# Kernel tuning notes

Hardware: AMD Instinct MI355X
Metric: run time of the kernel (lower is better)

The kernel has to match this reference:

```python
import jax, jax.numpy as jnp
import numpy as np

N, E = 50000, 800000
IN_F, OUT_F, EMB, KER = 64, 64, 3, 4


def setup_inputs() -> dict:
    key = jax.random.key(0)
    ks = jax.random.split(key, 6)
    x = jax.random.normal(ks[0], (N, IN_F), dtype=jnp.float32)
    edge_idx = jax.random.randint(ks[1], (2, E), 0, N, dtype=jnp.int64)
    spec_domain = jax.random.normal(ks[2], (N, EMB), dtype=jnp.float32)
    weight = 0.1 * jax.random.normal(ks[3], (IN_F, OUT_F, KER), dtype=jnp.float32)
    bias_p = 0.1 * jax.random.normal(ks[4], (OUT_F,), dtype=jnp.float32)
    mu = 0.005 * jax.random.normal(ks[5], (EMB, KER), dtype=jnp.float32)
    sig = jnp.ones((1, KER), dtype=jnp.float32)  # repo default 60140 underflows exp with random embeddings
    return {"x": x, "edge_idx": edge_idx, "spec_domain": spec_domain,
            "weight": weight, "bias_p": bias_p, "mu": mu, "sig": sig}


def reference(x, edge_idx, spec_domain, weight, bias_p, mu, sig):
    n = x.shape[0]
    row, col = edge_idx[0], edge_idx[1]
    # support for all kernels at once: [N, out, K]
    support = jnp.einsum('ni,iok->nok', x, weight)
    # per-edge Gaussian kernel values: [E, K]
    diff = spec_domain[row] - spec_domain[col]               # [E, emb]
    dm = diff[:, :, None] - mu[None, :, :]                   # [E, emb, K]
    qq = -0.5 * jnp.sum(dm * dm, axis=1)                     # [E, K]
    value = jnp.exp(sig[0][None, :] * qq)                    # [E, K]
    # sparse mm: out[row] += value * support[col], per kernel
    msgs = value[:, None, :] * support[col]                  # [E, out, K]
    out = jax.ops.segment_sum(msgs, row, num_segments=n)     # [N, out, K]
    return out.sum(axis=2) + bias_p
```

## Files before the change

### kernel.cpp

```cpp
#include <hip/hip_runtime.h>
#include <hip/hip_fp16.h>

#define FIN 64
#define CAP 64
#define BINSH 8
#define NBINMAX 256
#define PCAP 5120

__global__ __launch_bounds__(256) void p1_kernel(const float* __restrict__ x,
                                                 const float* __restrict__ weight,
                                                 __half* __restrict__ sup,
                                                 const int* __restrict__ eidx,
                                                 int* __restrict__ gcur,
                                                 int* __restrict__ part,
                                                 int n, int e_total) {
    const int t = threadIdx.x;
    __shared__ float xs[32][64];
    __shared__ int hist[NBINMAX], lbase[NBINMAX], gbase[NBINMAX];
    __shared__ int wsum[4];
    __shared__ int slds[512];

    const int rowbase = blockIdx.x * 32;
    if (rowbase < n) {
        {
            const float4* __restrict__ x4 = (const float4*)(x + (size_t)rowbase * 64);
            float4* __restrict__ s4 = (float4*)&xs[0][0];
            int limit = (n - rowbase) * 16;
            if (limit > 512) limit = 512;
            #pragma unroll
            for (int j = 0; j < 2; ++j) {
                int idx = t + j * 256;
                if (idx < limit) s4[idx] = x4[idx];
            }
        }
        __syncthreads();

        const int w = t >> 6;
        const int o = t & 63;

        float4 acc[8];
        #pragma unroll
        for (int r = 0; r < 8; ++r) acc[r] = make_float4(0.f, 0.f, 0.f, 0.f);

        #pragma unroll 4
        for (int ic = 0; ic < 16; ++ic) {
            float4 w0 = *(const float4*)&weight[(ic * 4 + 0) * 256 + o * 4];
            float4 w1 = *(const float4*)&weight[(ic * 4 + 1) * 256 + o * 4];
            float4 w2 = *(const float4*)&weight[(ic * 4 + 2) * 256 + o * 4];
            float4 w3 = *(const float4*)&weight[(ic * 4 + 3) * 256 + o * 4];
            #pragma unroll
            for (int r = 0; r < 8; ++r) {
                float4 xv = *(const float4*)&xs[w * 8 + r][ic * 4];
                acc[r].x += xv.x * w0.x + xv.y * w1.x + xv.z * w2.x + xv.w * w3.x;
                acc[r].y += xv.x * w0.y + xv.y * w1.y + xv.z * w2.y + xv.w * w3.y;
                acc[r].z += xv.x * w0.z + xv.y * w1.z + xv.z * w2.z + xv.w * w3.z;
                acc[r].w += xv.x * w0.w + xv.y * w1.w + xv.z * w2.w + xv.w * w3.w;
            }
        }

        #pragma unroll
        for (int r = 0; r < 8; ++r) {
            int gr = rowbase + w * 8 + r;
            if (gr < n) {
                union { __half2 h[2]; uint2 u; } p;
                p.h[0] = __floats2half2_rn(acc[r].x, acc[r].y);
                p.h[1] = __floats2half2_rn(acc[r].z, acc[r].w);
                *(uint2*)&sup[(size_t)gr * 256 + o * 4] = p.u;
            }
        }
    }

    int nz = 0;
    #pragma unroll
    for (int j = 1; j < 16; j += 2) nz |= eidx[j];
    const int is64 = (nz == 0);

    hist[t] = 0;
    __syncthreads();

    const int base = blockIdx.x * 512;
    const int nv = (e_total - base < 512) ? (e_total - base < 0 ? 0 : e_total - base)
                                          : 512;
    const int p = (base >> 1) + t;
    int r0 = 0, c0 = 0, r1 = 0, c1 = 0, v0 = 0, v1 = 0;
    if (nv > 0) {
        if (is64) {
            if (2 * t < nv) {
                int4 rr = ((const int4*)eidx)[p];
                int4 cc = ((const int4*)(eidx + 2 * (size_t)e_total))[p];
                r0 = rr.x; c0 = cc.x; v0 = 1;
                if (2 * t + 1 < nv) { r1 = rr.z; c1 = cc.z; v1 = 1; }
            }
        } else {
            if (2 * t < nv) {
                int2 rr = ((const int2*)eidx)[p];
                int2 cc = ((const int2*)(eidx + (size_t)e_total))[p];
                r0 = rr.x; c0 = cc.x; v0 = 1;
                if (2 * t + 1 < nv) { r1 = rr.y; c1 = cc.y; v1 = 1; }
            }
        }
    }
    const int b0 = r0 >> BINSH, b1 = r1 >> BINSH;
    int lp0 = 0, lp1 = 0;
    if (v0) lp0 = atomicAdd(&hist[b0], 1);
    if (v1) lp1 = atomicAdd(&hist[b1], 1);
    __syncthreads();

    {
        const int lane = t & 63;
        const int w = t >> 6;
        int h = hist[t];
        int s = h;
        #pragma unroll
        for (int off = 1; off < 64; off <<= 1) {
            int u = __shfl_up(s, off, 64);
            if (lane >= off) s += u;
        }
        if (lane == 63) wsum[w] = s;
        __syncthreads();
        if (t == 0) {
            int a = 0;
            #pragma unroll
            for (int q = 0; q < 4; ++q) { int u = wsum[q]; wsum[q] = a; a += u; }
        }
        __syncthreads();
        int ex = s - h + wsum[w];
        lbase[t] = ex;
        gbase[t] = (h > 0) ? atomicAdd(&gcur[t], h) : 0;
    }
    __syncthreads();

    if (v0) slds[lbase[b0] + lp0] = (b0 << 24) | (c0 << 8) | (r0 & 255);
    if (v1) slds[lbase[b1] + lp1] = (b1 << 24) | (c1 << 8) | (r1 & 255);
    __syncthreads();

    #pragma unroll
    for (int j = 0; j < 2; ++j) {
        int idx = t + j * 256;
        if (idx < nv) {
            int wv = slds[idx];
            int b = ((unsigned)wv) >> 24;
            int dst = gbase[b] + (idx - lbase[b]);
            if (dst < PCAP) part[b * PCAP + dst] = wv & 0x00FFFFFF;
        }
    }
}

__global__ __launch_bounds__(1024) void p2_kernel(const int* __restrict__ gcur,
                                                  const int* __restrict__ part,
                                                  int* __restrict__ cnt,
                                                  int* __restrict__ scol, int n) {
    __shared__ int cl[256];
    const int t = threadIdx.x;
    const int b = blockIdx.x;
    const int row0 = b << BINSH;
    if (t < 256) cl[t] = 0;
    __syncthreads();

    int nloc = gcur[b];
    if (nloc > PCAP) nloc = PCAP;
    const int* __restrict__ mypart = part + b * PCAP;

    for (int i = t; i < nloc; i += 1024) {
        int e = mypart[i];
        int rl = e & 255;
        int col = ((unsigned)e) >> 8;
        int pos = atomicAdd(&cl[rl], 1);
        if (pos < CAP) scol[(size_t)(row0 + rl) * CAP + pos] = col;
    }
    __syncthreads();

    int row = row0 + t;
    if (t < 256 && row < n) cnt[row] = cl[t];
}

__device__ __forceinline__ float dot_sup(uint2 p, float4 v) {
    float2 f0 = __half22float2(__builtin_bit_cast(__half2, p.x));
    float2 f1 = __half22float2(__builtin_bit_cast(__half2, p.y));
    return f0.x * v.x + f0.y * v.y + f1.x * v.z + f1.y * v.w;
}

__global__ __launch_bounds__(256, 8) void row_kernel(const int* __restrict__ cnt,
                                                     const int* __restrict__ scol,
                                                     const float* __restrict__ spec,
                                                     const float* __restrict__ mu,
                                                     const float* __restrict__ sig,
                                                     const __half* __restrict__ sup,
                                                     const float* __restrict__ bias,
                                                     float* __restrict__ out, int n) {
    __shared__ float vlds[4][64];
    const int lane = threadIdx.x & 63;
    const int wl = threadIdx.x >> 6;
    const int wv = __builtin_amdgcn_readfirstlane(blockIdx.x * 4 + wl);
    const int NW = gridDim.x * 4;

    const int k  = lane & 3;
    const int es = lane >> 2;
    const float mu0 = mu[k], mu1 = mu[4 + k], mu2 = mu[8 + k];
    const float sgk = sig[k];
    const float bias_l = bias[lane];
    const unsigned un = (unsigned)n;

    for (int r = wv; r < n; r += NW) {
        int ecount = cnt[r];
        if (ecount > CAP) ecount = CAP;
        const int base = r * CAP;
        const float sr0 = spec[r * 3 + 0];
        const float sr1 = spec[r * 3 + 1];
        const float sr2 = spec[r * 3 + 2];
        float acc = bias_l;

        for (int j = 0; j < ecount; j += 16) {
            int nb = ecount - j; if (nb > 16) nb = 16;

            float myv = 0.f;
            if (es < nb) {
                int mycol = scol[base + j + es];
                float d0 = sr0 - spec[mycol * 3 + 0];
                float d1 = sr1 - spec[mycol * 3 + 1];
                float d2 = sr2 - spec[mycol * 3 + 2];
                float a = d0 - mu0, b = d1 - mu1, c = d2 - mu2;
                myv = __expf(sgk * (-0.5f * (a * a + b * b + c * c)));
            }
            vlds[wl][lane] = myv;

            int nbr = (nb + 7) & ~7;
            for (int ee = 0; ee < nbr; ee += 8) {
                int c0 = scol[base + j + ee + 0];
                int c1 = scol[base + j + ee + 1];
                int c2 = scol[base + j + ee + 2];
                int c3 = scol[base + j + ee + 3];
                int c4 = scol[base + j + ee + 4];
                int c5 = scol[base + j + ee + 5];
                int c6 = scol[base + j + ee + 6];
                int c7 = scol[base + j + ee + 7];
                c0 = ((unsigned)c0 < un) ? c0 : 0;
                c1 = ((unsigned)c1 < un) ? c1 : 0;
                c2 = ((unsigned)c2 < un) ? c2 : 0;
                c3 = ((unsigned)c3 < un) ? c3 : 0;
                c4 = ((unsigned)c4 < un) ? c4 : 0;
                c5 = ((unsigned)c5 < un) ? c5 : 0;
                c6 = ((unsigned)c6 < un) ? c6 : 0;
                c7 = ((unsigned)c7 < un) ? c7 : 0;
                uint2 p0 = *(const uint2*)(sup + ((size_t)c0 * 256 + lane * 4));
                uint2 p1 = *(const uint2*)(sup + ((size_t)c1 * 256 + lane * 4));
                uint2 p2 = *(const uint2*)(sup + ((size_t)c2 * 256 + lane * 4));
                uint2 p3 = *(const uint2*)(sup + ((size_t)c3 * 256 + lane * 4));
                uint2 p4 = *(const uint2*)(sup + ((size_t)c4 * 256 + lane * 4));
                uint2 p5 = *(const uint2*)(sup + ((size_t)c5 * 256 + lane * 4));
                uint2 p6 = *(const uint2*)(sup + ((size_t)c6 * 256 + lane * 4));
                uint2 p7 = *(const uint2*)(sup + ((size_t)c7 * 256 + lane * 4));
                float4 v0 = *(const float4*)&vlds[wl][(ee + 0) * 4];
                float4 v1 = *(const float4*)&vlds[wl][(ee + 1) * 4];
                float4 v2 = *(const float4*)&vlds[wl][(ee + 2) * 4];
                float4 v3 = *(const float4*)&vlds[wl][(ee + 3) * 4];
                float4 v4 = *(const float4*)&vlds[wl][(ee + 4) * 4];
                float4 v5 = *(const float4*)&vlds[wl][(ee + 5) * 4];
                float4 v6 = *(const float4*)&vlds[wl][(ee + 6) * 4];
                float4 v7 = *(const float4*)&vlds[wl][(ee + 7) * 4];
                acc += dot_sup(p0, v0);
                acc += dot_sup(p1, v1);
                acc += dot_sup(p2, v2);
                acc += dot_sup(p3, v3);
                acc += dot_sup(p4, v4);
                acc += dot_sup(p5, v5);
                acc += dot_sup(p6, v6);
                acc += dot_sup(p7, v7);
            }
        }
        out[(size_t)r * 64 + lane] = acc;
    }
}

extern "C" void kernel_launch(void* const* d_in, const int* in_sizes, int n_in,
                              void* d_out, int out_size, void* d_ws, size_t ws_size,
                              hipStream_t stream) {
    const float* x      = (const float*)d_in[0];
    const int*   eidx   = (const int*)d_in[1];
    const float* spec   = (const float*)d_in[2];
    const float* weight = (const float*)d_in[3];
    const float* bias   = (const float*)d_in[4];
    const float* mu     = (const float*)d_in[5];
    const float* sig    = (const float*)d_in[6];
    float* out = (float*)d_out;

    const int N = in_sizes[0] / FIN;
    const int E = in_sizes[1] / 2;
    const int NB32 = (N + 31) / 32;
    const int NTILE = (E + 511) / 512;
    const int GRID1 = (NB32 > NTILE) ? NB32 : NTILE;
    const int NBIN = (N + (1 << BINSH) - 1) >> BINSH;

    char* w = (char*)d_ws;
    size_t off = 0;
    int* gcur = (int*)(w + off);            off += NBINMAX * 4;
    __half* sup = (__half*)(w + off);       off += (size_t)N * 256 * sizeof(__half);
    off = (off + 255) & ~(size_t)255;
    int* cnt = (int*)(w + off);             off += (size_t)N * 4;
    off = (off + 255) & ~(size_t)255;
    int* scol = (int*)(w + off);            off += (size_t)N * CAP * 4;
    off = (off + 255) & ~(size_t)255;
    int* part = (int*)(w + off);            off += (size_t)NBIN * PCAP * 4;

    hipMemsetAsync(gcur, 0, NBINMAX * 4, stream);
    p1_kernel<<<GRID1, 256, 0, stream>>>(x, weight, sup, eidx, gcur, part, N, E);
    p2_kernel<<<NBIN, 1024, 0, stream>>>(gcur, part, cnt, scol, N);
    row_kernel<<<2048, 256, 0, stream>>>(cnt, scol, spec, mu, sig, sup, bias, out, N);
}
```

Before: 126.3 us.

## Split fused support/sort kernel into two kernels and retune row kernel occupancy

The combined p1 kernel that computed the fp16 support matrix and binned the edges is split into a separate support_kernel and sort_kernel. The new support kernel reads x straight from global memory with wave-uniform loads instead of staging it in shared memory, and keeps 8 weight rows in registers per step. The row kernel's launch bound goes from 8 to 6 waves per SIMD and its grid from 2048 to 1536 blocks. This removes the shared-memory staging and the mixed workload per block, at the cost of one extra launch and of running the two phases one after the other instead of inside the same blocks.

```diff
diff --git a/kernel.cpp b/kernel.cpp
--- a/kernel.cpp
+++ b/kernel.cpp
@@ -7,68 +7,71 @@
 #define NBINMAX 256
 #define PCAP 5120
 
-__global__ __launch_bounds__(256) void p1_kernel(const float* __restrict__ x,
-                                                 const float* __restrict__ weight,
-                                                 __half* __restrict__ sup,
-                                                 const int* __restrict__ eidx,
-                                                 int* __restrict__ gcur,
-                                                 int* __restrict__ part,
-                                                 int n, int e_total) {
+__global__ __launch_bounds__(256) void support_kernel(const float* __restrict__ x,
+                                                      const float* __restrict__ weight,
+                                                      __half* __restrict__ sup, int n) {
+    const int lane = threadIdx.x & 63;
+    const int wid  = threadIdx.x >> 6;
+    const int r0 = blockIdx.x * 32 + wid * 8;
+    if (r0 >= n) return;
+    const int nr = (n - r0 < 8) ? (n - r0) : 8;
+    const float* __restrict__ xr = x + (size_t)r0 * 64;
+
+    float4 acc[8];
+    #pragma unroll
+    for (int r = 0; r < 8; ++r) acc[r] = make_float4(0.f, 0.f, 0.f, 0.f);
+
+    for (int ib = 0; ib < 8; ++ib) {
+        float4 wreg[8];
+        #pragma unroll
+        for (int q = 0; q < 8; ++q)
+            wreg[q] = *(const float4*)&weight[(ib * 8 + q) * 256 + lane * 4];
+
+        if (nr == 8) {
+            #pragma unroll
+            for (int rr = 0; rr < 8; ++rr) {
+                #pragma unroll
+                for (int q = 0; q < 8; ++q) {
+                    float xv = xr[rr * 64 + ib * 8 + q];
+                    acc[rr].x += xv * wreg[q].x;
+                    acc[rr].y += xv * wreg[q].y;
+                    acc[rr].z += xv * wreg[q].z;
+                    acc[rr].w += xv * wreg[q].w;
+                }
+            }
+        } else {
+            for (int rr = 0; rr < nr; ++rr) {
+                #pragma unroll
+                for (int q = 0; q < 8; ++q) {
+                    float xv = xr[rr * 64 + ib * 8 + q];
+                    acc[rr].x += xv * wreg[q].x;
+                    acc[rr].y += xv * wreg[q].y;
+                    acc[rr].z += xv * wreg[q].z;
+                    acc[rr].w += xv * wreg[q].w;
+                }
+            }
+        }
+    }
+
+    #pragma unroll
+    for (int r = 0; r < 8; ++r) {
+        if (r < nr) {
+            union { __half2 h[2]; uint2 u; } p;
+            p.h[0] = __floats2half2_rn(acc[r].x, acc[r].y);
+            p.h[1] = __floats2half2_rn(acc[r].z, acc[r].w);
+            *(uint2*)&sup[(size_t)(r0 + r) * 256 + lane * 4] = p.u;
+        }
+    }
+}
+
+__global__ __launch_bounds__(256) void sort_kernel(const int* __restrict__ eidx,
+                                                   int* __restrict__ gcur,
+                                                   int* __restrict__ part,
+                                                   int e_total) {
     const int t = threadIdx.x;
-    __shared__ float xs[32][64];
     __shared__ int hist[NBINMAX], lbase[NBINMAX], gbase[NBINMAX];
     __shared__ int wsum[4];
     __shared__ int slds[512];
-
-    const int rowbase = blockIdx.x * 32;
-    if (rowbase < n) {
-        {
-            const float4* __restrict__ x4 = (const float4*)(x + (size_t)rowbase * 64);
-            float4* __restrict__ s4 = (float4*)&xs[0][0];
-            int limit = (n - rowbase) * 16;
-            if (limit > 512) limit = 512;
-            #pragma unroll
-            for (int j = 0; j < 2; ++j) {
-                int idx = t + j * 256;
-                if (idx < limit) s4[idx] = x4[idx];
-            }
-        }
-        __syncthreads();
-
-        const int w = t >> 6;
-        const int o = t & 63;
-
-        float4 acc[8];
-        #pragma unroll
-        for (int r = 0; r < 8; ++r) acc[r] = make_float4(0.f, 0.f, 0.f, 0.f);
-
-        #pragma unroll 4
-        for (int ic = 0; ic < 16; ++ic) {
-            float4 w0 = *(const float4*)&weight[(ic * 4 + 0) * 256 + o * 4];
-            float4 w1 = *(const float4*)&weight[(ic * 4 + 1) * 256 + o * 4];
-            float4 w2 = *(const float4*)&weight[(ic * 4 + 2) * 256 + o * 4];
-            float4 w3 = *(const float4*)&weight[(ic * 4 + 3) * 256 + o * 4];
-            #pragma unroll
-            for (int r = 0; r < 8; ++r) {
-                float4 xv = *(const float4*)&xs[w * 8 + r][ic * 4];
-                acc[r].x += xv.x * w0.x + xv.y * w1.x + xv.z * w2.x + xv.w * w3.x;
-                acc[r].y += xv.x * w0.y + xv.y * w1.y + xv.z * w2.y + xv.w * w3.y;
-                acc[r].z += xv.x * w0.z + xv.y * w1.z + xv.z * w2.z + xv.w * w3.z;
-                acc[r].w += xv.x * w0.w + xv.y * w1.w + xv.z * w2.w + xv.w * w3.w;
-            }
-        }
-
-        #pragma unroll
-        for (int r = 0; r < 8; ++r) {
-            int gr = rowbase + w * 8 + r;
-            if (gr < n) {
-                union { __half2 h[2]; uint2 u; } p;
-                p.h[0] = __floats2half2_rn(acc[r].x, acc[r].y);
-                p.h[1] = __floats2half2_rn(acc[r].z, acc[r].w);
-                *(uint2*)&sup[(size_t)gr * 256 + o * 4] = p.u;
-            }
-        }
-    }
 
     int nz = 0;
     #pragma unroll
@@ -124,8 +127,7 @@
             for (int q = 0; q < 4; ++q) { int u = wsum[q]; wsum[q] = a; a += u; }
         }
         __syncthreads();
-        int ex = s - h + wsum[w];
-        lbase[t] = ex;
+        lbase[t] = s - h + wsum[w];
         gbase[t] = (h > 0) ? atomicAdd(&gcur[t], h) : 0;
     }
     __syncthreads();
@@ -180,7 +182,7 @@
     return f0.x * v.x + f0.y * v.y + f1.x * v.z + f1.y * v.w;
 }
 
-__global__ __launch_bounds__(256, 8) void row_kernel(const int* __restrict__ cnt,
+__global__ __launch_bounds__(256, 6) void row_kernel(const int* __restrict__ cnt,
                                                      const int* __restrict__ scol,
                                                      const float* __restrict__ spec,
                                                      const float* __restrict__ mu,
@@ -288,7 +290,6 @@
     const int E = in_sizes[1] / 2;
     const int NB32 = (N + 31) / 32;
     const int NTILE = (E + 511) / 512;
-    const int GRID1 = (NB32 > NTILE) ? NB32 : NTILE;
     const int NBIN = (N + (1 << BINSH) - 1) >> BINSH;
 
     char* w = (char*)d_ws;
@@ -303,7 +304,8 @@
     int* part = (int*)(w + off);            off += (size_t)NBIN * PCAP * 4;
 
     hipMemsetAsync(gcur, 0, NBINMAX * 4, stream);
-    p1_kernel<<<GRID1, 256, 0, stream>>>(x, weight, sup, eidx, gcur, part, N, E);
+    support_kernel<<<NB32, 256, 0, stream>>>(x, weight, sup, N);
+    sort_kernel<<<NTILE, 256, 0, stream>>>(eidx, gcur, part, E);
     p2_kernel<<<NBIN, 1024, 0, stream>>>(gcur, part, cnt, scol, N);
-    row_kernel<<<2048, 256, 0, stream>>>(cnt, scol, spec, mu, sig, sup, bias, out, N);
-}
+    row_kernel<<<1536, 256, 0, stream>>>(cnt, scol, spec, mu, sig, sup, bias, out, N);
+}
```

Result: slower. 263.3 us (+108.5%).
